# Optimization experiments

Measured on AMD Instinct MI355X. Metric: run time of the kernel, lower is better.

Reference implementation:

```python
import jax, jax.numpy as jnp
import numpy as np

EPS = 1.1920929e-07  # torch.finfo(float32).eps, used by F.rms_norm default

def rope(x, cos, sin):
    # x: [B,T,H,D]; cos/sin: [1,T,1,D//2]
    d = x.shape[-1] // 2
    x1, x2 = x[..., :d], x[..., d:]
    return jnp.concatenate([x1 * cos + x2 * sin, -x1 * sin + x2 * cos], axis=-1)

def rmsnorm(x):
    return x * jax.lax.rsqrt(jnp.mean(x * x, axis=-1, keepdims=True) + EPS)

def setup_inputs() -> dict:
    key = jax.random.key(0)
    ks = jax.random.split(key, 9)
    B, T, E = 2, 2048, 1024
    Hkv, D = 4, 64
    return {
        "x": jax.random.normal(ks[0], (B, T, E), jnp.float32),
        "ve": jax.random.normal(ks[1], (B, T, Hkv * D), jnp.float32),
        "cos": jax.random.normal(ks[2], (1, T, 1, D // 2), jnp.float32),
        "sin": jax.random.normal(ks[3], (1, T, 1, D // 2), jnp.float32),
        "Wq": jax.random.normal(ks[4], (E, E), jnp.float32) * 0.02,
        "Wk": jax.random.normal(ks[5], (Hkv * D, E), jnp.float32) * 0.02,
        "Wv": jax.random.normal(ks[6], (Hkv * D, E), jnp.float32) * 0.02,
        "Wproj": jax.random.normal(ks[7], (E, E), jnp.float32) * 0.02,
        "Wgate": jax.random.normal(ks[8], (Hkv, 32), jnp.float32) * 0.02,
        "window_size": 1024,
    }

def reference(x, ve, cos, sin, Wq, Wk, Wv, Wproj, Wgate, window_size):
    B, T, E = x.shape
    H, Hkv, D = 16, 4, 64
    G = H // Hkv  # GQA group size
    q = (x @ Wq.T).reshape(B, T, H, D)
    k = (x @ Wk.T).reshape(B, T, Hkv, D)
    v = (x @ Wv.T).reshape(B, T, Hkv, D)
    # value-embedding gating
    gate = 2.0 * jax.nn.sigmoid(x[..., :32] @ Wgate.T)          # [B,T,Hkv]
    v = v + gate[..., None] * ve.reshape(B, T, Hkv, D)
    # RoPE then QK RMS-norm
    q = rmsnorm(rope(q, cos, sin))
    k = rmsnorm(rope(k, cos, sin))
    # to [B,H,T,D]; repeat-interleave kv heads for GQA (matches torch enable_gqa)
    q = q.transpose(0, 2, 1, 3)
    k = jnp.repeat(k.transpose(0, 2, 1, 3), G, axis=1)
    v = jnp.repeat(v.transpose(0, 2, 1, 3), G, axis=1)
    # causal + sliding-window boolean mask
    row = jnp.arange(T)[:, None]
    col = jnp.arange(T)[None, :]
    mask = (col <= row) & (col >= row - window_size)            # [T,T]
    scale = 1.0 / jnp.sqrt(jnp.float32(D))
    scores = jnp.einsum("bhqd,bhkd->bhqk", q, k) * scale
    scores = jnp.where(mask, scores, -jnp.inf)
    p = jax.nn.softmax(scores, axis=-1)
    y = jnp.einsum("bhqk,bhkd->bhqd", p, v)
    y = y.transpose(0, 2, 1, 3).reshape(B, T, E)
    return y @ Wproj.T
```

## Files before the change

### kernel.cpp

```cpp
#include <hip/hip_runtime.h>


typedef float f32x4 __attribute__((ext_vector_type(4)));
typedef short s16x8 __attribute__((ext_vector_type(8)));
typedef short s16x4 __attribute__((ext_vector_type(4)));
typedef _Float16 f16x4 __attribute__((ext_vector_type(4)));

__device__ __forceinline__ unsigned short f2bf(float f) {
  unsigned u = __float_as_uint(f);
  u += 0x7fffu + ((u >> 16) & 1u);
  return (unsigned short)(u >> 16);
}
__device__ __forceinline__ unsigned short h16(float f) {
  _Float16 h = (_Float16)f;
  return __builtin_bit_cast(unsigned short, h);
}

__device__ __forceinline__ float fexp2(float x) {
#if __has_builtin(__builtin_amdgcn_exp2f)
  return __builtin_amdgcn_exp2f(x);
#else
  return __expf(x * 0.69314718f);
#endif
}

__device__ __forceinline__ void gl2lds16(const unsigned short* g, unsigned short* l) {
  __builtin_amdgcn_global_load_lds((const __attribute__((address_space(1))) unsigned int*)g,
                                   (__attribute__((address_space(3))) unsigned int*)l, 16, 0, 0);
}

__global__ __launch_bounds__(256) void cvt_gate(
    const float* __restrict__ x, const float* __restrict__ wq, const float* __restrict__ wk,
    const float* __restrict__ wv, const float* __restrict__ wp, const float* __restrict__ wgate,
    unsigned short* __restrict__ xb, unsigned short* __restrict__ wqkv,
    unsigned short* __restrict__ wpj, float* __restrict__ gatep) {
  int blk = blockIdx.x;
  if (blk < 6656) {
    int i = blk * 256 + threadIdx.x;
    const float* s;
    unsigned short* d;
    if (i < 1048576) { s = x; d = xb; }
    else if (i < 1310720) { i -= 1048576; s = wq; d = wqkv; }
    else if (i < 1376256) { i -= 1310720; s = wk; d = wqkv + 1048576; }
    else if (i < 1441792) { i -= 1376256; s = wv; d = wqkv + 1310720; }
    else { i -= 1441792; s = wp; d = wpj; }
    float4 v = ((const float4*)s)[i];
    ushort4 o;
    o.x = f2bf(v.x); o.y = f2bf(v.y); o.z = f2bf(v.z); o.w = f2bf(v.w);
    ((ushort4*)d)[i] = o;
  } else {
    int i = (blk - 6656) * 256 + threadIdx.x;
    int bt = i >> 2, h = i & 3;
    const float4* xp = (const float4*)(x + (size_t)bt * 1024);
    const float4* wpt = (const float4*)(wgate + h * 32);
    float s = 0.f;
#pragma unroll
    for (int j = 0; j < 8; ++j) {
      float4 a = xp[j], b = wpt[j];
      s += a.x * b.x + a.y * b.y + a.z * b.z + a.w * b.w;
    }
    gatep[i] = 2.f / (1.f + __expf(-s));
  }
}

__global__ __launch_bounds__(256) void gemm_qkv(
    const unsigned short* __restrict__ A, const unsigned short* __restrict__ B,
    const float* __restrict__ cosp, const float* __restrict__ sinp,
    const float* __restrict__ gatep, const float* __restrict__ ve,
    unsigned short* __restrict__ q_r, unsigned short* __restrict__ k_r,
    unsigned short* __restrict__ vp2) {
  __shared__ unsigned short smem[24576];
  unsigned short* As = smem;
  unsigned short* Bs = smem + 8192;
  const int K = 1024;
  int lin = blockIdx.y * 12 + blockIdx.x;
  int nl = (lin & 7) * 96 + (lin >> 3);
  int bn = nl % 12, bm = nl / 12;
  int t = threadIdx.x;
  int w = t >> 6, lane = t & 63;
  int c = lane & 15, g = lane >> 4;
  int wm = w >> 1, wn = w & 1;

  f32x4 acc[2][4];
#pragma unroll
  for (int i = 0; i < 2; ++i)
#pragma unroll
    for (int j = 0; j < 4; ++j) acc[i][j] = (f32x4){0.f, 0.f, 0.f, 0.f};

  const unsigned short* Ab = A + (size_t)(bm * 64) * K;
  const unsigned short* Bb = B + (size_t)(bn * 128) * K;
  int srow = lane >> 4;
  int sgrp = lane & 15;

  for (int k0 = 0; k0 < K; k0 += 128) {
#pragma unroll
    for (int j = 0; j < 4; ++j) {
      int r0 = w * 16 + j * 4;
      int r = r0 + srow;
      gl2lds16(Ab + (size_t)r * K + k0 + (sgrp ^ (r & 7)) * 8, As + r0 * 128);
    }
#pragma unroll
    for (int j = 0; j < 8; ++j) {
      int r0 = w * 32 + j * 4;
      int r = r0 + srow;
      gl2lds16(Bb + (size_t)r * K + k0 + (sgrp ^ (r & 7)) * 8, Bs + r0 * 128);
    }
    __syncthreads();
#pragma unroll
    for (int kk = 0; kk < 4; ++kk) {
      int sw = ((kk * 4 + g) ^ (c & 7)) * 8;
      s16x8 af[2], bf[4];
#pragma unroll
      for (int mt = 0; mt < 2; ++mt)
        af[mt] = *(const s16x8*)(As + (wm * 32 + mt * 16 + c) * 128 + sw);
#pragma unroll
      for (int nt = 0; nt < 4; ++nt)
        bf[nt] = *(const s16x8*)(Bs + (wn * 64 + nt * 16 + c) * 128 + sw);
#pragma unroll
      for (int mt = 0; mt < 2; ++mt)
#pragma unroll
        for (int nt = 0; nt < 4; ++nt)
          acc[mt][nt] = __builtin_amdgcn_mfma_f32_16x16x32_bf16(af[mt], bf[nt], acc[mt][nt], 0, 0, 0);
    }
    __syncthreads();
  }

  const float QSCL = 0.125f * 1.44269504f;
  if (bn < 10) {
    unsigned short* eb = smem + w * 2176;
#pragma unroll
    for (int mt = 0; mt < 2; ++mt) {
#pragma unroll
      for (int r = 0; r < 4; ++r) {
        int lrow = mt * 16 + g * 4 + r;
        int rowg = bm * 64 + wm * 32 + lrow;
        int tt = rowg & 2047;
        float v0 = acc[mt][0][r], v1 = acc[mt][1][r], v2 = acc[mt][2][r], v3 = acc[mt][3][r];
        float cs0 = cosp[tt * 32 + c], sn0 = sinp[tt * 32 + c];
        float cs1 = cosp[tt * 32 + 16 + c], sn1 = sinp[tt * 32 + 16 + c];
        float r0 = v0 * cs0 + v2 * sn0;
        float r1 = v1 * cs1 + v3 * sn1;
        float r2 = v2 * cs0 - v0 * sn0;
        float r3 = v3 * cs1 - v1 * sn1;
        float ss = r0 * r0 + r1 * r1 + r2 * r2 + r3 * r3;
        ss += __shfl_xor(ss, 1);
        ss += __shfl_xor(ss, 2);
        ss += __shfl_xor(ss, 4);
        ss += __shfl_xor(ss, 8);
        float sc = rsqrtf(ss * (1.0f / 64.0f) + 1.1920929e-07f);
        if (bn < 8) sc *= QSCL;
        eb[lrow * 68 + c] = f2bf(r0 * sc);
        eb[lrow * 68 + 16 + c] = f2bf(r1 * sc);
        eb[lrow * 68 + 32 + c] = f2bf(r2 * sc);
        eb[lrow * 68 + 48 + c] = f2bf(r3 * sc);
      }
    }
    asm volatile("s_waitcnt lgkmcnt(0)" ::: "memory");
#pragma unroll
    for (int j = 0; j < 4; ++j) {
      int idx = lane * 4 + j;
      int lrow = idx >> 3;
      int ck = idx & 7;
      s16x8 val = *(const s16x8*)(eb + lrow * 68 + ck * 8);
      int rowg = bm * 64 + wm * 32 + lrow;
      int b = rowg >> 11, tt = rowg & 2047;
      unsigned short* dst;
      if (bn < 8) dst = q_r + ((size_t)(b * 16 + bn * 2 + wn) * 2048 + tt) * 64 + ck * 8;
      else dst = k_r + ((size_t)(b * 4 + (bn - 8) * 2 + wn) * 2048 + tt) * 64 + ck * 8;
      *(s16x8*)dst = val;
    }
  } else {
    unsigned short* eb = smem + w * 2560;
    int h = (bn - 10) * 2 + wn;
#pragma unroll
    for (int mt = 0; mt < 2; ++mt) {
#pragma unroll
      for (int r = 0; r < 4; ++r) {
        int key = mt * 16 + g * 4 + r;
        int rowg = bm * 64 + wm * 32 + key;
        float gate = gatep[rowg * 4 + h];
        const float* vep = ve + (size_t)rowg * 256 + h * 64;
        eb[(0 * 16 + c) * 40 + key] = h16(acc[mt][0][r] + gate * vep[c]);
        eb[(1 * 16 + c) * 40 + key] = h16(acc[mt][1][r] + gate * vep[16 + c]);
        eb[(2 * 16 + c) * 40 + key] = h16(acc[mt][2][r] + gate * vep[32 + c]);
        eb[(3 * 16 + c) * 40 + key] = h16(acc[mt][3][r] + gate * vep[48 + c]);
      }
    }
    asm volatile("s_waitcnt lgkmcnt(0)" ::: "memory");
    int rowg0 = bm * 64 + wm * 32;
    int b = rowg0 >> 11;
    int tile = (rowg0 & 2047) >> 5;
    unsigned short* vb = vp2 + ((size_t)(b * 4 + h) * 64 + tile) * 2048;
#pragma unroll
    for (int j = 0; j < 4; ++j) {
      int cid = j * 64 + lane;
      int d = cid >> 2;
      int kg = cid & 3;
      s16x8 val = *(const s16x8*)(eb + d * 40 + kg * 8);
      *(s16x8*)(vb + d * 32 + kg * 8) = val;
    }
  }
}

__global__ __launch_bounds__(256) void gemm_bf16_128(
    const unsigned short* __restrict__ A, const unsigned short* __restrict__ B,
    float* __restrict__ C, int K, int ldc) {
  __shared__ unsigned short As[2][128 * 128];
  __shared__ unsigned short Bs[2][128 * 128];
  int lin = blockIdx.y * 8 + blockIdx.x;
  int nl = (lin & 7) * 32 + (lin >> 3);
  int bn = nl & 7, bm = nl >> 3;
  int t = threadIdx.x;
  int w = t >> 6, lane = t & 63;
  int c = lane & 15, g = lane >> 4;
  int wm = w >> 1, wn = w & 1;

  f32x4 acc[4][4];
#pragma unroll
  for (int i = 0; i < 4; ++i)
#pragma unroll
    for (int j = 0; j < 4; ++j) acc[i][j] = (f32x4){0.f, 0.f, 0.f, 0.f};

  const unsigned short* Ab = A + (size_t)(bm * 128) * K;
  const unsigned short* Bb = B + (size_t)(bn * 128) * K;
  int srow = lane >> 4;
  int sgrp = lane & 15;

#define STAGE128(buf, k0)                                                          \
  {                                                                                \
    _Pragma("unroll")                                                              \
    for (int j = 0; j < 8; ++j) {                                                  \
      int r0 = w * 32 + j * 4;                                                     \
      int r = r0 + srow;                                                           \
      gl2lds16(Ab + (size_t)r * K + (k0) + (sgrp ^ (r & 7)) * 8, &As[buf][r0 * 128]); \
      gl2lds16(Bb + (size_t)r * K + (k0) + (sgrp ^ (r & 7)) * 8, &Bs[buf][r0 * 128]); \
    }                                                                              \
  }

  STAGE128(0, 0);
  for (int tstep = 0; tstep < 8; ++tstep) {
    int buf = tstep & 1;
    __syncthreads();
    if (tstep < 7) STAGE128(buf ^ 1, (tstep + 1) * 128);
#pragma unroll
    for (int kk = 0; kk < 4; ++kk) {
      int sw = ((kk * 4 + g) ^ (c & 7)) * 8;
      s16x8 af[4], bf[4];
#pragma unroll
      for (int mt = 0; mt < 4; ++mt)
        af[mt] = *(const s16x8*)(&As[buf][(wm * 64 + mt * 16 + c) * 128 + sw]);
#pragma unroll
      for (int nt = 0; nt < 4; ++nt)
        bf[nt] = *(const s16x8*)(&Bs[buf][(wn * 64 + nt * 16 + c) * 128 + sw]);
#pragma unroll
      for (int mt = 0; mt < 4; ++mt)
#pragma unroll
        for (int nt = 0; nt < 4; ++nt)
          acc[mt][nt] = __builtin_amdgcn_mfma_f32_16x16x32_bf16(af[mt], bf[nt], acc[mt][nt], 0, 0, 0);
    }
  }
#undef STAGE128

#pragma unroll
  for (int mt = 0; mt < 4; ++mt)
#pragma unroll
    for (int nt = 0; nt < 4; ++nt)
#pragma unroll
      for (int r = 0; r < 4; ++r) {
        int rowg = bm * 128 + wm * 64 + mt * 16 + g * 4 + r;
        int colg = bn * 128 + wn * 64 + nt * 16 + c;
        C[(size_t)rowg * ldc + colg] = acc[mt][nt][r];
      }
}

__global__ __launch_bounds__(256) void attn_kernel(
    const unsigned short* __restrict__ q_r, const unsigned short* __restrict__ k_r,
    const unsigned short* __restrict__ v_p2, unsigned short* __restrict__ y_b,
    const int* __restrict__ wptr) {
  const int W = *wptr;
  const int bid = blockIdx.x;
  const int rr = bid >> 8, cc = bid & 255;
  const int mm = cc & 7;
  const int h = (cc >> 3) & 15, b = cc >> 7;
  const int qt = (rr == 0) ? mm : (rr == 1) ? 15 - mm : (rr == 2) ? 16 + mm : 31 - mm;
  const int tid = threadIdx.x;
  const int w = tid >> 6, lane = tid & 63, c = lane & 15, g = lane >> 4;
  const int r0b = qt * 64;
  const int r0w = r0b + w * 16;
  const int hkv = h >> 2;
  const float M = 11.5415603f;

  __shared__ unsigned short Ks[2][32 * 68];
  __shared__ unsigned short Vs[2][64 * 40];

  const unsigned short* kbase = k_r + (size_t)(b * 4 + hkv) * 131072;
  const unsigned short* vbase = v_p2 + (size_t)(b * 4 + hkv) * 131072;
  const unsigned short* qbase = q_r + ((size_t)(b * 16 + h) * 2048 + r0w) * 64;

  s16x8 q_lo = *(const s16x8*)(qbase + c * 64 + g * 8);
  s16x8 q_hi = *(const s16x8*)(qbase + c * 64 + 32 + g * 8);

  int kt0w = r0w - W; if (kt0w < 0) kt0w = 0;
  const int ktEw = r0w + 16;
  int KT0 = r0b - W; if (KT0 < 0) KT0 = 0;
  KT0 &= ~31;
  const int KTE = r0b + 64;

  float l_part = 0.f;
  f32x4 acc[4];
#pragma unroll
  for (int dt = 0; dt < 4; ++dt) acc[dt] = (f32x4){0.f, 0.f, 0.f, 0.f};

  s16x8 pk = *(const s16x8*)(kbase + (size_t)KT0 * 64 + tid * 8);
  s16x8 pv = *(const s16x8*)(vbase + (size_t)(KT0 >> 5) * 2048 + tid * 8);

  const int koff = (tid >> 3) * 68 + (tid & 7) * 8;
  const int voff = (tid >> 2) * 40 + (tid & 3) * 8;

  int bufI = 0;
  for (int kt = KT0; kt < KTE; kt += 32, bufI ^= 1) {
    int nkt = (kt + 32 < KTE) ? kt + 32 : kt;
    s16x8 nk = *(const s16x8*)(kbase + (size_t)nkt * 64 + tid * 8);
    s16x8 nv = *(const s16x8*)(vbase + (size_t)(nkt >> 5) * 2048 + tid * 8);

    unsigned short* kdst = &Ks[bufI][koff];
    *(s16x4*)kdst = __builtin_shufflevector(pk, pk, 0, 1, 2, 3);
    *(s16x4*)(kdst + 4) = __builtin_shufflevector(pk, pk, 4, 5, 6, 7);
    *(s16x8*)(&Vs[bufI][voff]) = pv;
    __syncthreads();

    if (kt + 32 > kt0w && kt < ktEw) {
      const unsigned short* kr0 = &Ks[bufI][c * 68 + g * 8];
      s16x4 a0 = *(const s16x4*)(kr0);
      s16x4 a1 = *(const s16x4*)(kr0 + 4);
      s16x4 a2 = *(const s16x4*)(kr0 + 32);
      s16x4 a3 = *(const s16x4*)(kr0 + 36);
      const unsigned short* kr1 = kr0 + 16 * 68;
      s16x4 a4 = *(const s16x4*)(kr1);
      s16x4 a5 = *(const s16x4*)(kr1 + 4);
      s16x4 a6 = *(const s16x4*)(kr1 + 32);
      s16x4 a7 = *(const s16x4*)(kr1 + 36);
      s16x8 k0lo = __builtin_shufflevector(a0, a1, 0, 1, 2, 3, 4, 5, 6, 7);
      s16x8 k0hi = __builtin_shufflevector(a2, a3, 0, 1, 2, 3, 4, 5, 6, 7);
      s16x8 k1lo = __builtin_shufflevector(a4, a5, 0, 1, 2, 3, 4, 5, 6, 7);
      s16x8 k1hi = __builtin_shufflevector(a6, a7, 0, 1, 2, 3, 4, 5, 6, 7);

      f32x4 S0 = (f32x4){0.f, 0.f, 0.f, 0.f};
      f32x4 S1 = (f32x4){0.f, 0.f, 0.f, 0.f};
      S0 = __builtin_amdgcn_mfma_f32_16x16x32_bf16(k0lo, q_lo, S0, 0, 0, 0);
      S0 = __builtin_amdgcn_mfma_f32_16x16x32_bf16(k0hi, q_hi, S0, 0, 0, 0);
      S1 = __builtin_amdgcn_mfma_f32_16x16x32_bf16(k1lo, q_lo, S1, 0, 0, 0);
      S1 = __builtin_amdgcn_mfma_f32_16x16x32_bf16(k1hi, q_hi, S1, 0, 0, 0);

      f16x4 P0, P1;
      const bool edge = (kt < kt0w + 32) || (kt + 32 > r0w);
      const int qrow = r0w + c;
#pragma unroll
      for (int r = 0; r < 4; ++r) {
        float p0 = fexp2(S0[r] - M);
        float p1 = fexp2(S1[r] - M);
        if (edge) {
          int k0i = kt + g * 4 + r;
          int k1i = k0i + 16;
          if (!(k0i <= qrow && k0i >= qrow - W)) p0 = 0.f;
          if (!(k1i <= qrow && k1i >= qrow - W)) p1 = 0.f;
        }
        l_part += p0 + p1;
        P0[r] = (_Float16)p0;
        P1[r] = (_Float16)p1;
      }

#pragma unroll
      for (int dt = 0; dt < 4; ++dt) {
        const unsigned short* vr = &Vs[bufI][(dt * 16 + c) * 40 + g * 4];
        f16x4 va = *(const f16x4*)(vr);
        f16x4 vb = *(const f16x4*)(vr + 16);
        acc[dt] = __builtin_amdgcn_mfma_f32_16x16x16f16(va, P0, acc[dt], 0, 0, 0);
        acc[dt] = __builtin_amdgcn_mfma_f32_16x16x16f16(vb, P1, acc[dt], 0, 0, 0);
      }
    }
    pk = nk; pv = nv;
  }

  float l = l_part;
  l += __shfl_xor(l, 16);
  l += __shfl_xor(l, 32);
  float inv = 1.0f / l;

  unsigned short* ob = y_b + ((size_t)(b * 2048 + r0w + c) * 16 + h) * 64 + g * 4;
#pragma unroll
  for (int dt = 0; dt < 4; ++dt) {
    ushort4 o;
    o.x = f2bf(acc[dt][0] * inv);
    o.y = f2bf(acc[dt][1] * inv);
    o.z = f2bf(acc[dt][2] * inv);
    o.w = f2bf(acc[dt][3] * inv);
    *(ushort4*)(ob + dt * 16) = o;
  }
}

extern "C" void kernel_launch(void* const* d_in, const int* in_sizes, int n_in,
                              void* d_out, int out_size, void* d_ws, size_t ws_size,
                              hipStream_t stream) {
  const float* x = (const float*)d_in[0];
  const float* ve = (const float*)d_in[1];
  const float* cosp = (const float*)d_in[2];
  const float* sinp = (const float*)d_in[3];
  const float* Wq = (const float*)d_in[4];
  const float* Wk = (const float*)d_in[5];
  const float* Wv = (const float*)d_in[6];
  const float* Wproj = (const float*)d_in[7];
  const float* Wgate = (const float*)d_in[8];
  const int* wptr = (const int*)d_in[9];

  unsigned short* xb = (unsigned short*)d_ws;
  unsigned short* wqkv = xb + 4194304;
  unsigned short* wpj = wqkv + 1572864;
  unsigned short* q_r = wpj + 1048576;
  unsigned short* k_r = q_r + 4194304;
  unsigned short* y_b = k_r + 1048576;
  unsigned short* vp2 = y_b + 4194304;
  float* gatep = (float*)(vp2 + 1048576);

  cvt_gate<<<6720, 256, 0, stream>>>(x, Wq, Wk, Wv, Wproj, Wgate, xb, wqkv, wpj, gatep);
  gemm_qkv<<<dim3(12, 64), 256, 0, stream>>>(xb, wqkv, cosp, sinp, gatep, ve, q_r, k_r, vp2);
  attn_kernel<<<1024, 256, 0, stream>>>(q_r, k_r, vp2, y_b, wptr);
  gemm_bf16_128<<<dim3(8, 32), 256, 0, stream>>>(y_b, wpj, (float*)d_out, 1024, 1024);
}
```

Before: 165.8 us.

## Process all four GQA query heads per attention block to reuse K/V tiles

Each attention block now computes all four query heads that share one KV head, loading each K/V tile into shared memory once and reusing it for four heads' MFMA work. The grid shrinks from 1024 to 256 blocks and the block-to-tile mapping is reworked. This cuts redundant K/V global loads and LDS staging, at the cost of far more accumulator registers, lower occupancy, and a single wave of blocks with uneven per-block work across query tiles.

Result: slower. 190.1 us (+14.6%).

```diff
diff --git a/kernel.cpp b/kernel.cpp
--- a/kernel.cpp
+++ b/kernel.cpp
@@ -278,16 +278,15 @@
     const unsigned short* __restrict__ v_p2, unsigned short* __restrict__ y_b,
     const int* __restrict__ wptr) {
   const int W = *wptr;
-  const int bid = blockIdx.x;
-  const int rr = bid >> 8, cc = bid & 255;
-  const int mm = cc & 7;
-  const int h = (cc >> 3) & 15, b = cc >> 7;
-  const int qt = (rr == 0) ? mm : (rr == 1) ? 15 - mm : (rr == 2) ? 16 + mm : 31 - mm;
+  const int bid0 = blockIdx.x;
+  const int bid = (bid0 & 7) * 32 + (bid0 >> 3);
+  const int qt = bid & 31;
+  const int hkv = (bid >> 5) & 3;
+  const int b = bid >> 7;
   const int tid = threadIdx.x;
   const int w = tid >> 6, lane = tid & 63, c = lane & 15, g = lane >> 4;
   const int r0b = qt * 64;
   const int r0w = r0b + w * 16;
-  const int hkv = h >> 2;
   const float M = 11.5415603f;
 
   __shared__ unsigned short Ks[2][32 * 68];
@@ -295,10 +294,15 @@
 
   const unsigned short* kbase = k_r + (size_t)(b * 4 + hkv) * 131072;
   const unsigned short* vbase = v_p2 + (size_t)(b * 4 + hkv) * 131072;
-  const unsigned short* qbase = q_r + ((size_t)(b * 16 + h) * 2048 + r0w) * 64;
-
-  s16x8 q_lo = *(const s16x8*)(qbase + c * 64 + g * 8);
-  s16x8 q_hi = *(const s16x8*)(qbase + c * 64 + 32 + g * 8);
+
+  s16x8 q_lo[4], q_hi[4];
+#pragma unroll
+  for (int hh = 0; hh < 4; ++hh) {
+    const unsigned short* qbase =
+        q_r + ((size_t)(b * 16 + hkv * 4 + hh) * 2048 + r0w) * 64;
+    q_lo[hh] = *(const s16x8*)(qbase + c * 64 + g * 8);
+    q_hi[hh] = *(const s16x8*)(qbase + c * 64 + 32 + g * 8);
+  }
 
   int kt0w = r0w - W; if (kt0w < 0) kt0w = 0;
   const int ktEw = r0w + 16;
@@ -306,16 +310,19 @@
   KT0 &= ~31;
   const int KTE = r0b + 64;
 
-  float l_part = 0.f;
-  f32x4 acc[4];
-#pragma unroll
-  for (int dt = 0; dt < 4; ++dt) acc[dt] = (f32x4){0.f, 0.f, 0.f, 0.f};
+  float l_part[4] = {0.f, 0.f, 0.f, 0.f};
+  f32x4 acc[4][4];
+#pragma unroll
+  for (int hh = 0; hh < 4; ++hh)
+#pragma unroll
+    for (int dt = 0; dt < 4; ++dt) acc[hh][dt] = (f32x4){0.f, 0.f, 0.f, 0.f};
 
   s16x8 pk = *(const s16x8*)(kbase + (size_t)KT0 * 64 + tid * 8);
   s16x8 pv = *(const s16x8*)(vbase + (size_t)(KT0 >> 5) * 2048 + tid * 8);
 
   const int koff = (tid >> 3) * 68 + (tid & 7) * 8;
   const int voff = (tid >> 2) * 40 + (tid & 3) * 8;
+  const int qrow = r0w + c;
 
   int bufI = 0;
   for (int kt = KT0; kt < KTE; kt += 32, bufI ^= 1) {
@@ -345,57 +352,70 @@
       s16x8 k1lo = __builtin_shufflevector(a4, a5, 0, 1, 2, 3, 4, 5, 6, 7);
       s16x8 k1hi = __builtin_shufflevector(a6, a7, 0, 1, 2, 3, 4, 5, 6, 7);
 
-      f32x4 S0 = (f32x4){0.f, 0.f, 0.f, 0.f};
-      f32x4 S1 = (f32x4){0.f, 0.f, 0.f, 0.f};
-      S0 = __builtin_amdgcn_mfma_f32_16x16x32_bf16(k0lo, q_lo, S0, 0, 0, 0);
-      S0 = __builtin_amdgcn_mfma_f32_16x16x32_bf16(k0hi, q_hi, S0, 0, 0, 0);
-      S1 = __builtin_amdgcn_mfma_f32_16x16x32_bf16(k1lo, q_lo, S1, 0, 0, 0);
-      S1 = __builtin_amdgcn_mfma_f32_16x16x32_bf16(k1hi, q_hi, S1, 0, 0, 0);
-
-      f16x4 P0, P1;
-      const bool edge = (kt < kt0w + 32) || (kt + 32 > r0w);
-      const int qrow = r0w + c;
-#pragma unroll
-      for (int r = 0; r < 4; ++r) {
-        float p0 = fexp2(S0[r] - M);
-        float p1 = fexp2(S1[r] - M);
-        if (edge) {
-          int k0i = kt + g * 4 + r;
-          int k1i = k0i + 16;
-          if (!(k0i <= qrow && k0i >= qrow - W)) p0 = 0.f;
-          if (!(k1i <= qrow && k1i >= qrow - W)) p1 = 0.f;
-        }
-        l_part += p0 + p1;
-        P0[r] = (_Float16)p0;
-        P1[r] = (_Float16)p1;
-      }
-
+      f16x4 vfa[4], vfb[4];
 #pragma unroll
       for (int dt = 0; dt < 4; ++dt) {
         const unsigned short* vr = &Vs[bufI][(dt * 16 + c) * 40 + g * 4];
-        f16x4 va = *(const f16x4*)(vr);
-        f16x4 vb = *(const f16x4*)(vr + 16);
-        acc[dt] = __builtin_amdgcn_mfma_f32_16x16x16f16(va, P0, acc[dt], 0, 0, 0);
-        acc[dt] = __builtin_amdgcn_mfma_f32_16x16x16f16(vb, P1, acc[dt], 0, 0, 0);
+        vfa[dt] = *(const f16x4*)(vr);
+        vfb[dt] = *(const f16x4*)(vr + 16);
       }
+
+      const bool edge = (kt < kt0w + 32) || (kt + 32 > r0w);
+
+#pragma unroll
+      for (int hh = 0; hh < 4; ++hh) {
+        f32x4 S0 = (f32x4){0.f, 0.f, 0.f, 0.f};
+        f32x4 S1 = (f32x4){0.f, 0.f, 0.f, 0.f};
+        S0 = __builtin_amdgcn_mfma_f32_16x16x32_bf16(k0lo, q_lo[hh], S0, 0, 0, 0);
+        S0 = __builtin_amdgcn_mfma_f32_16x16x32_bf16(k0hi, q_hi[hh], S0, 0, 0, 0);
+        S1 = __builtin_amdgcn_mfma_f32_16x16x32_bf16(k1lo, q_lo[hh], S1, 0, 0, 0);
+        S1 = __builtin_amdgcn_mfma_f32_16x16x32_bf16(k1hi, q_hi[hh], S1, 0, 0, 0);
+
+        f16x4 P0, P1;
+        float lp = 0.f;
+#pragma unroll
+        for (int r = 0; r < 4; ++r) {
+          float p0 = fexp2(S0[r] - M);
+          float p1 = fexp2(S1[r] - M);
+          if (edge) {
+            int k0i = kt + g * 4 + r;
+            int k1i = k0i + 16;
+            if (!(k0i <= qrow && k0i >= qrow - W)) p0 = 0.f;
+            if (!(k1i <= qrow && k1i >= qrow - W)) p1 = 0.f;
+          }
+          lp += p0 + p1;
+          P0[r] = (_Float16)p0;
+          P1[r] = (_Float16)p1;
+        }
+        l_part[hh] += lp;
+
+#pragma unroll
+        for (int dt = 0; dt < 4; ++dt) {
+          acc[hh][dt] = __builtin_amdgcn_mfma_f32_16x16x16f16(vfa[dt], P0, acc[hh][dt], 0, 0, 0);
+          acc[hh][dt] = __builtin_amdgcn_mfma_f32_16x16x16f16(vfb[dt], P1, acc[hh][dt], 0, 0, 0);
+        }
+      }
     }
     pk = nk; pv = nv;
   }
 
-  float l = l_part;
-  l += __shfl_xor(l, 16);
-  l += __shfl_xor(l, 32);
-  float inv = 1.0f / l;
-
-  unsigned short* ob = y_b + ((size_t)(b * 2048 + r0w + c) * 16 + h) * 64 + g * 4;
-#pragma unroll
-  for (int dt = 0; dt < 4; ++dt) {
-    ushort4 o;
-    o.x = f2bf(acc[dt][0] * inv);
-    o.y = f2bf(acc[dt][1] * inv);
-    o.z = f2bf(acc[dt][2] * inv);
-    o.w = f2bf(acc[dt][3] * inv);
-    *(ushort4*)(ob + dt * 16) = o;
+#pragma unroll
+  for (int hh = 0; hh < 4; ++hh) {
+    float l = l_part[hh];
+    l += __shfl_xor(l, 16);
+    l += __shfl_xor(l, 32);
+    float inv = 1.0f / l;
+    unsigned short* ob =
+        y_b + ((size_t)(b * 2048 + r0w + c) * 16 + hkv * 4 + hh) * 64 + g * 4;
+#pragma unroll
+    for (int dt = 0; dt < 4; ++dt) {
+      ushort4 o;
+      o.x = f2bf(acc[hh][dt][0] * inv);
+      o.y = f2bf(acc[hh][dt][1] * inv);
+      o.z = f2bf(acc[hh][dt][2] * inv);
+      o.w = f2bf(acc[hh][dt][3] * inv);
+      *(ushort4*)(ob + dt * 16) = o;
+    }
   }
 }
 
@@ -424,6 +444,6 @@
 
   cvt_gate<<<6720, 256, 0, stream>>>(x, Wq, Wk, Wv, Wproj, Wgate, xb, wqkv, wpj, gatep);
   gemm_qkv<<<dim3(12, 64), 256, 0, stream>>>(xb, wqkv, cosp, sinp, gatep, ve, q_r, k_r, vp2);
-  attn_kernel<<<1024, 256, 0, stream>>>(q_r, k_r, vp2, y_b, wptr);
+  attn_kernel<<<256, 256, 0, stream>>>(q_r, k_r, vp2, y_b, wptr);
   gemm_bf16_128<<<dim3(8, 32), 256, 0, stream>>>(y_b, wpj, (float*)d_out, 1024, 1024);
 }
```

## Share K/V tiles across the four GQA query heads in one 1024-thread block

Applied to the files above, without the earlier changes.

The attention kernel now launches 256 blocks of 1024 threads, each covering one KV head and one 64-row query tile. Its 16 waves handle 4 query heads × 4 row groups, so each K/V tile is loaded into shared memory once per GQA group instead of once per query head. This cuts global and LDS traffic for K/V by a factor of four. In exchange, blocks are larger and fewer, the causal load-balancing tile order is replaced by a simpler block remap, and per-block barriers now synchronise 16 waves.

Result: slower. 170.0 us (+2.5%).

```diff
diff --git a/kernel.cpp b/kernel.cpp
--- a/kernel.cpp
+++ b/kernel.cpp
@@ -273,21 +273,22 @@
       }
 }
 
-__global__ __launch_bounds__(256) void attn_kernel(
+__global__ __launch_bounds__(1024) void attn_kernel(
     const unsigned short* __restrict__ q_r, const unsigned short* __restrict__ k_r,
     const unsigned short* __restrict__ v_p2, unsigned short* __restrict__ y_b,
     const int* __restrict__ wptr) {
   const int W = *wptr;
-  const int bid = blockIdx.x;
-  const int rr = bid >> 8, cc = bid & 255;
-  const int mm = cc & 7;
-  const int h = (cc >> 3) & 15, b = cc >> 7;
-  const int qt = (rr == 0) ? mm : (rr == 1) ? 15 - mm : (rr == 2) ? 16 + mm : 31 - mm;
+  const int bid0 = blockIdx.x;
+  const int bid = (bid0 & 7) * 32 + (bid0 >> 3);
+  const int qt = bid & 31;
+  const int hkv = (bid >> 5) & 3;
+  const int b = bid >> 7;
   const int tid = threadIdx.x;
   const int w = tid >> 6, lane = tid & 63, c = lane & 15, g = lane >> 4;
+  const int wq = w & 3, wh = w >> 2;
   const int r0b = qt * 64;
-  const int r0w = r0b + w * 16;
-  const int hkv = h >> 2;
+  const int r0w = r0b + wq * 16;
+  const int h = hkv * 4 + wh;
   const float M = 11.5415603f;
 
   __shared__ unsigned short Ks[2][32 * 68];
@@ -311,22 +312,31 @@
 #pragma unroll
   for (int dt = 0; dt < 4; ++dt) acc[dt] = (f32x4){0.f, 0.f, 0.f, 0.f};
 
-  s16x8 pk = *(const s16x8*)(kbase + (size_t)KT0 * 64 + tid * 8);
-  s16x8 pv = *(const s16x8*)(vbase + (size_t)(KT0 >> 5) * 2048 + tid * 8);
-
-  const int koff = (tid >> 3) * 68 + (tid & 7) * 8;
-  const int voff = (tid >> 2) * 40 + (tid & 3) * 8;
+  const bool isK = tid < 512;
+  const int kkey = tid >> 4, kcg = (tid & 15) * 4;
+  const int vj = tid - 512;
+  const int ldsOff = isK ? (kkey * 68 + kcg) : ((vj >> 3) * 40 + (vj & 7) * 4);
+
+  s16x4 pfr;
+  {
+    const unsigned short* src = isK
+        ? (kbase + (size_t)(KT0 + kkey) * 64 + kcg)
+        : (vbase + (size_t)(KT0 >> 5) * 2048 + vj * 4);
+    pfr = *(const s16x4*)src;
+  }
+
+  const int qrow = r0w + c;
 
   int bufI = 0;
   for (int kt = KT0; kt < KTE; kt += 32, bufI ^= 1) {
     int nkt = (kt + 32 < KTE) ? kt + 32 : kt;
-    s16x8 nk = *(const s16x8*)(kbase + (size_t)nkt * 64 + tid * 8);
-    s16x8 nv = *(const s16x8*)(vbase + (size_t)(nkt >> 5) * 2048 + tid * 8);
-
-    unsigned short* kdst = &Ks[bufI][koff];
-    *(s16x4*)kdst = __builtin_shufflevector(pk, pk, 0, 1, 2, 3);
-    *(s16x4*)(kdst + 4) = __builtin_shufflevector(pk, pk, 4, 5, 6, 7);
-    *(s16x8*)(&Vs[bufI][voff]) = pv;
+    const unsigned short* nsrc = isK
+        ? (kbase + (size_t)(nkt + kkey) * 64 + kcg)
+        : (vbase + (size_t)(nkt >> 5) * 2048 + vj * 4);
+    s16x4 nfr = *(const s16x4*)nsrc;
+
+    unsigned short* dst = isK ? &Ks[bufI][ldsOff] : &Vs[bufI][ldsOff];
+    *(s16x4*)dst = pfr;
     __syncthreads();
 
     if (kt + 32 > kt0w && kt < ktEw) {
@@ -354,7 +364,6 @@
 
       f16x4 P0, P1;
       const bool edge = (kt < kt0w + 32) || (kt + 32 > r0w);
-      const int qrow = r0w + c;
 #pragma unroll
       for (int r = 0; r < 4; ++r) {
         float p0 = fexp2(S0[r] - M);
@@ -379,7 +388,7 @@
         acc[dt] = __builtin_amdgcn_mfma_f32_16x16x16f16(vb, P1, acc[dt], 0, 0, 0);
       }
     }
-    pk = nk; pv = nv;
+    pfr = nfr;
   }
 
   float l = l_part;
@@ -424,6 +433,6 @@
 
   cvt_gate<<<6720, 256, 0, stream>>>(x, Wq, Wk, Wv, Wproj, Wgate, xb, wqkv, wpj, gatep);
   gemm_qkv<<<dim3(12, 64), 256, 0, stream>>>(xb, wqkv, cosp, sinp, gatep, ve, q_r, k_r, vp2);
-  attn_kernel<<<1024, 256, 0, stream>>>(q_r, k_r, vp2, y_b, wptr);
+  attn_kernel<<<256, 1024, 0, stream>>>(q_r, k_r, vp2, y_b, wptr);
   gemm_bf16_128<<<dim3(8, 32), 256, 0, stream>>>(y_b, wpj, (float*)d_out, 1024, 1024);
 }
```
